# Kernel optimization log

Hardware: AMD Instinct MI355X
Metric: run time of the kernel (lower is better)

Reference implementation:

```python
import jax, jax.numpy as jnp
import numpy as np

N = 50000        # nodes
E = 800000       # edges (avg degree 16)
H = 128          # hidden_channels
R = 6            # num_radial
SH = 3           # spin_hidden_channels


def _linear_params(key, out_dim, in_dim):
    # torch Linear default init: U(-1/sqrt(in), 1/sqrt(in)) for weight and bias
    kw, kb = jax.random.split(key)
    bound = 1.0 / np.sqrt(in_dim)
    W = jax.random.uniform(kw, (out_dim, in_dim), minval=-bound, maxval=bound, dtype=jnp.float32)
    b = jax.random.uniform(kb, (out_dim,), minval=-bound, maxval=bound, dtype=jnp.float32)
    return W, b


def setup_inputs() -> dict:
    key = jax.random.key(0)
    ks = jax.random.split(key, 9)
    x = jax.random.randint(ks[0], (N,), 0, 95)                       # atom types
    s = jax.random.randint(ks[1], (N,), 0, 3)                        # spin class in {0,1,2} == (spin + 1)
    rbf = jax.random.normal(ks[2], (E, R), dtype=jnp.float32)
    i = jax.random.randint(ks[3], (E,), 0, N)
    j = jax.random.randint(ks[4], (E,), 0, N)
    emb_w = jax.random.uniform(ks[5], (95, H), minval=-np.sqrt(3), maxval=np.sqrt(3), dtype=jnp.float32)
    spin_w, spin_b = _linear_params(ks[6], SH, 3)
    rbf_w, rbf_b = _linear_params(ks[7], H, R)
    lin_w, lin_b = _linear_params(ks[8], H, 3 * H + 2 * SH)
    return {"x": x, "s": s, "rbf": rbf, "i": i, "j": j,
            "emb_w": emb_w, "spin_w": spin_w, "spin_b": spin_b,
            "rbf_w": rbf_w, "rbf_b": rbf_b, "lin_w": lin_w, "lin_b": lin_b}


def reference(x, s, rbf, i, j, emb_w, spin_w, spin_b, rbf_w, rbf_b, lin_w, lin_b):
    act = jax.nn.silu
    h = emb_w[x]                                              # [N, H] embedding lookup
    spin_oh = jax.nn.one_hot(s, 3, dtype=spin_w.dtype)        # [N, 3]
    spin_feat = spin_oh @ spin_w.T + spin_b                   # [N, SH]
    r = act(rbf @ rbf_w.T + rbf_b)                            # [E, H]
    # concat order matches torch: [x_i, spin_i, x_j, spin_j, rbf]
    feat = jnp.concatenate([h[i], spin_feat[i], h[j], spin_feat[j], r], axis=-1)  # [E, 3H+2SH]
    return act(feat @ lin_w.T + lin_b)                        # [E, H]
```

## Files before the change

### kernel.cpp

```cpp
#include <hip/hip_runtime.h>
#include <hip/hip_bf16.h>

#define NH   128
#define NR   6
#define NCOL 390
#define TILE_E 128
#define LDK  136
#define NBLK 512

typedef __attribute__((ext_vector_type(8))) short bf16x8;
typedef __attribute__((ext_vector_type(4))) float f32x4;

__device__ __forceinline__ float fast_silu(float v) {
    return v * __builtin_amdgcn_rcpf(1.0f + __expf(-v));
}

__global__ void prep_tables(const float* __restrict__ emb_w,
                            const float* __restrict__ spin_w,
                            const float* __restrict__ spin_b,
                            const float* __restrict__ lin_w,
                            const float* __restrict__ lin_b,
                            float* __restrict__ Ci, float* __restrict__ Cj) {
    int row = blockIdx.x;
    int n   = threadIdx.x;
    bool isJ = row >= 285;
    int rr = isJ ? row - 285 : row;
    int a  = rr / 3;
    int sc = rr % 3;
    const int col0 = isJ ? 131 : 0;
    const int cols = isJ ? 259 : 128;
    const float* wrow = lin_w + (size_t)n * NCOL;
    float acc = isJ ? 0.0f : lin_b[n];
    #pragma unroll 8
    for (int k = 0; k < NH; ++k)
        acc += emb_w[a * NH + k] * wrow[col0 + k];
    #pragma unroll
    for (int c = 0; c < 3; ++c)
        acc += (spin_w[c * 3 + sc] + spin_b[c]) * wrow[cols + c];
    (isJ ? Cj : Ci)[rr * NH + n] = acc;
}

__global__ void prep_w(const float* __restrict__ lin_w, __hip_bfloat16* __restrict__ Wb) {
    int idx = blockIdx.x * 256 + threadIdx.x;
    int n = idx >> 7, k = idx & 127;
    Wb[idx] = __float2bfloat16(lin_w[(size_t)n * NCOL + 262 + k]);
}

__global__ __launch_bounds__(512, 4) void fused_main(
        const int*   __restrict__ x,   const int* __restrict__ s,
        const float* __restrict__ rbf,
        const int*   __restrict__ gi,  const int* __restrict__ gj,
        const float* __restrict__ rbf_w, const float* __restrict__ rbf_b,
        const float* __restrict__ Ci,  const float* __restrict__ Cj,
        const __hip_bfloat16* __restrict__ Wb,
        float* __restrict__ out, int E, int ntiles) {
    __shared__ __align__(16) __hip_bfloat16 w_lds[NH * LDK];
    __shared__ __align__(16) __hip_bfloat16 r_lds[TILE_E * LDK];
    __shared__ float rbf_lds[TILE_E * NR];
    __shared__ int ci_lds[TILE_E], cj_lds[TILE_E];

    const int tid = threadIdx.x;

    float2 srbf = make_float2(0.f, 0.f);
    int sci = 0, scj = 0;

    auto load_tile = [&](int tt) {
        const int en0 = tt * TILE_E;
        if (tid < 384) {
            int nval = (E - en0 >= TILE_E ? TILE_E : E - en0) * NR;
            float2 v = make_float2(0.f, 0.f);
            if (tid * 2 < nval)
                v = ((const float2*)(rbf + (size_t)en0 * NR))[tid];
            srbf = v;
        }
        if (tid >= 384) {
            int e = en0 + (tid - 384); if (e >= E) e = E - 1;
            int ii = gi[e];
            sci = x[ii] * 3 + s[ii];
        }
        if (tid < 128) {
            int e = en0 + tid; if (e >= E) e = E - 1;
            int jj = gj[e];
            scj = x[jj] * 3 + s[jj];
        }
    };

    const int t0 = blockIdx.x;
    const int gstride = gridDim.x;
    load_tile(t0);

    {
        const uint4* src = (const uint4*)Wb;
        #pragma unroll
        for (int it = 0; it < 4; ++it) {
            int l = it * 512 + tid;
            uint4 v = src[l];
            *(uint4*)&w_lds[(l >> 4) * LDK + (l & 15) * 8] = v;
        }
    }

    const int kk = tid & 127;
    const int hi = tid >> 7;
    const float w0 = rbf_w[kk * NR + 0], w1 = rbf_w[kk * NR + 1], w2 = rbf_w[kk * NR + 2];
    const float w3 = rbf_w[kk * NR + 3], w4 = rbf_w[kk * NR + 4], w5 = rbf_w[kk * NR + 5];
    const float bb = rbf_b[kk];

    const int wave   = tid >> 6;
    const int lane   = tid & 63;
    const int lane15 = lane & 15;
    const int quad   = lane >> 4;
    const int e_sub  = wave * 16;
    const int e_row  = e_sub + quad * 4;

    for (int t = t0; t < ntiles; t += gstride) {
        __syncthreads();
        if (tid < 384) ((float2*)rbf_lds)[tid] = srbf;
        if (tid >= 384) ci_lds[tid - 384] = sci;
        if (tid < 128)  cj_lds[tid] = scj;
        __syncthreads();

        #pragma unroll 4
        for (int it = 0; it < 32; ++it) {
            int e = it * 4 + hi;
            const float* re = &rbf_lds[e * NR];
            float a = bb + re[0] * w0 + re[1] * w1 + re[2] * w2
                         + re[3] * w3 + re[4] * w4 + re[5] * w5;
            r_lds[e * LDK + kk] = __float2bfloat16(fast_silu(a));
        }
        __syncthreads();

        bf16x8 afrag[4];
        #pragma unroll
        for (int kt = 0; kt < 4; ++kt)
            afrag[kt] = *(const bf16x8*)&r_lds[(e_sub + lane15) * LDK + kt * 32 + quad * 8];

        const int e0 = t * TILE_E;
        const float* cip[4]; const float* cjp[4]; float* op[4];
        #pragma unroll
        for (int reg = 0; reg < 4; ++reg) {
            cip[reg] = Ci + ci_lds[e_row + reg] * NH + lane15;
            cjp[reg] = Cj + cj_lds[e_row + reg] * NH + lane15;
            op[reg]  = out + (size_t)(e0 + e_row + reg) * NH + lane15;
        }
        const bool tail = (e0 + TILE_E > E);

        int tn = t + gstride;
        if (tn < ntiles) load_tile(tn);

        #pragma unroll
        for (int nt = 0; nt < 8; ++nt) {
            f32x4 acc = {0.f, 0.f, 0.f, 0.f};
            #pragma unroll
            for (int kt = 0; kt < 4; ++kt) {
                bf16x8 bfrag = *(const bf16x8*)&w_lds[(nt * 16 + lane15) * LDK + kt * 32 + quad * 8];
                acc = __builtin_amdgcn_mfma_f32_16x16x32_bf16(afrag[kt], bfrag, acc, 0, 0, 0);
            }
            #pragma unroll
            for (int reg = 0; reg < 4; ++reg) {
                float base = cip[reg][nt * 16] + cjp[reg][nt * 16];
                float v = acc[reg] + base;
                float sv = fast_silu(v);
                if (!tail || (e0 + e_row + reg < E))
                    __builtin_nontemporal_store(sv, op[reg] + nt * 16);
            }
        }
    }
}

extern "C" void kernel_launch(void* const* d_in, const int* in_sizes, int n_in,
                              void* d_out, int out_size, void* d_ws, size_t ws_size,
                              hipStream_t stream) {
    const int*   x      = (const int*)  d_in[0];
    const int*   s      = (const int*)  d_in[1];
    const float* rbf    = (const float*)d_in[2];
    const int*   gi     = (const int*)  d_in[3];
    const int*   gj     = (const int*)  d_in[4];
    const float* emb_w  = (const float*)d_in[5];
    const float* spin_w = (const float*)d_in[6];
    const float* spin_b = (const float*)d_in[7];
    const float* rbf_w  = (const float*)d_in[8];
    const float* rbf_b  = (const float*)d_in[9];
    const float* lin_w  = (const float*)d_in[10];
    const float* lin_b  = (const float*)d_in[11];
    const int E = in_sizes[3];

    float* Ci = (float*)d_ws;
    float* Cj = Ci + 285 * NH;
    __hip_bfloat16* Wb = (__hip_bfloat16*)(Cj + 285 * NH);

    prep_tables<<<570, 128, 0, stream>>>(emb_w, spin_w, spin_b, lin_w, lin_b, Ci, Cj);
    prep_w<<<64, 256, 0, stream>>>(lin_w, Wb);

    int ntiles = (E + TILE_E - 1) / TILE_E;
    int nblk = ntiles < NBLK ? ntiles : NBLK;
    fused_main<<<nblk, 512, 0, stream>>>(x, s, rbf, gi, gj, rbf_w, rbf_b,
                                         Ci, Cj, Wb, (float*)d_out, E, ntiles);
}
```

Measured before the change: 553.9 us.

## Merge prep kernels and read rbf directly from global with register prefetch

Combines the two preprocessing kernels into one launch, and each block now computes the shared embedding dot product once for all three spin classes. In the main kernel the rbf staging through LDS is removed. Each wave reads its edge's six rbf values straight from global memory (wave-uniform addresses, next row prefetched into registers), which drops one barrier per tile. The cost is that rbf loads now sit on the critical path with no cross-tile prefetch.

```diff
diff --git a/kernel.cpp b/kernel.cpp
--- a/kernel.cpp
+++ b/kernel.cpp
@@ -15,35 +15,41 @@
     return v * __builtin_amdgcn_rcpf(1.0f + __expf(-v));
 }
 
-__global__ void prep_tables(const float* __restrict__ emb_w,
-                            const float* __restrict__ spin_w,
-                            const float* __restrict__ spin_b,
-                            const float* __restrict__ lin_w,
-                            const float* __restrict__ lin_b,
-                            float* __restrict__ Ci, float* __restrict__ Cj) {
-    int row = blockIdx.x;
-    int n   = threadIdx.x;
-    bool isJ = row >= 285;
-    int rr = isJ ? row - 285 : row;
-    int a  = rr / 3;
-    int sc = rr % 3;
-    const int col0 = isJ ? 131 : 0;
-    const int cols = isJ ? 259 : 128;
+__global__ void prep_all(const float* __restrict__ emb_w,
+                         const float* __restrict__ spin_w,
+                         const float* __restrict__ spin_b,
+                         const float* __restrict__ lin_w,
+                         const float* __restrict__ lin_b,
+                         float* __restrict__ Ci, float* __restrict__ Cj,
+                         __hip_bfloat16* __restrict__ Wb) {
+    int b = blockIdx.x;
+    int tid = threadIdx.x;
+    if (b >= 190) {
+        int idx = (b - 190) * 128 + tid;
+        int n = idx >> 7, k = idx & 127;
+        Wb[idx] = __float2bfloat16(lin_w[(size_t)n * NCOL + 262 + k]);
+        return;
+    }
+    int side = b & 1;
+    int a    = b >> 1;
+    int n    = tid;
+    const int col0 = side ? 131 : 0;
+    const int cols = side ? 259 : 128;
     const float* wrow = lin_w + (size_t)n * NCOL;
-    float acc = isJ ? 0.0f : lin_b[n];
+    const float* ew   = emb_w + a * NH;
+    float dot = side ? 0.0f : lin_b[n];
     #pragma unroll 8
     for (int k = 0; k < NH; ++k)
-        acc += emb_w[a * NH + k] * wrow[col0 + k];
+        dot += ew[k] * wrow[col0 + k];
+    float* dst = (side ? Cj : Ci) + (size_t)(a * 3) * NH + n;
     #pragma unroll
-    for (int c = 0; c < 3; ++c)
-        acc += (spin_w[c * 3 + sc] + spin_b[c]) * wrow[cols + c];
-    (isJ ? Cj : Ci)[rr * NH + n] = acc;
-}
-
-__global__ void prep_w(const float* __restrict__ lin_w, __hip_bfloat16* __restrict__ Wb) {
-    int idx = blockIdx.x * 256 + threadIdx.x;
-    int n = idx >> 7, k = idx & 127;
-    Wb[idx] = __float2bfloat16(lin_w[(size_t)n * NCOL + 262 + k]);
+    for (int sc = 0; sc < 3; ++sc) {
+        float acc = dot;
+        #pragma unroll
+        for (int c = 0; c < 3; ++c)
+            acc += (spin_w[c * 3 + sc] + spin_b[c]) * wrow[cols + c];
+        dst[(size_t)sc * NH] = acc;
+    }
 }
 
 __global__ __launch_bounds__(512, 4) void fused_main(
@@ -56,23 +62,13 @@
         float* __restrict__ out, int E, int ntiles) {
     __shared__ __align__(16) __hip_bfloat16 w_lds[NH * LDK];
     __shared__ __align__(16) __hip_bfloat16 r_lds[TILE_E * LDK];
-    __shared__ float rbf_lds[TILE_E * NR];
     __shared__ int ci_lds[TILE_E], cj_lds[TILE_E];
 
     const int tid = threadIdx.x;
 
-    float2 srbf = make_float2(0.f, 0.f);
     int sci = 0, scj = 0;
-
-    auto load_tile = [&](int tt) {
+    auto load_idx = [&](int tt) {
         const int en0 = tt * TILE_E;
-        if (tid < 384) {
-            int nval = (E - en0 >= TILE_E ? TILE_E : E - en0) * NR;
-            float2 v = make_float2(0.f, 0.f);
-            if (tid * 2 < nval)
-                v = ((const float2*)(rbf + (size_t)en0 * NR))[tid];
-            srbf = v;
-        }
         if (tid >= 384) {
             int e = en0 + (tid - 384); if (e >= E) e = E - 1;
             int ii = gi[e];
@@ -87,7 +83,7 @@
 
     const int t0 = blockIdx.x;
     const int gstride = gridDim.x;
-    load_tile(t0);
+    load_idx(t0);
 
     {
         const uint4* src = (const uint4*)Wb;
@@ -100,7 +96,7 @@
     }
 
     const int kk = tid & 127;
-    const int hi = tid >> 7;
+    const int hiu = __builtin_amdgcn_readfirstlane(tid >> 7);
     const float w0 = rbf_w[kk * NR + 0], w1 = rbf_w[kk * NR + 1], w2 = rbf_w[kk * NR + 2];
     const float w3 = rbf_w[kk * NR + 3], w4 = rbf_w[kk * NR + 4], w5 = rbf_w[kk * NR + 5];
     const float bb = rbf_b[kk];
@@ -113,19 +109,26 @@
     const int e_row  = e_sub + quad * 4;
 
     for (int t = t0; t < ntiles; t += gstride) {
+        const int e0t = t * TILE_E;
         __syncthreads();
-        if (tid < 384) ((float2*)rbf_lds)[tid] = srbf;
         if (tid >= 384) ci_lds[tid - 384] = sci;
         if (tid < 128)  cj_lds[tid] = scj;
-        __syncthreads();
 
-        #pragma unroll 4
-        for (int it = 0; it < 32; ++it) {
-            int e = it * 4 + hi;
-            const float* re = &rbf_lds[e * NR];
-            float a = bb + re[0] * w0 + re[1] * w1 + re[2] * w2
-                         + re[3] * w3 + re[4] * w4 + re[5] * w5;
-            r_lds[e * LDK + kk] = __float2bfloat16(fast_silu(a));
+        {
+            const int egBase = e0t + hiu * 32;
+            int eg0 = egBase; if (eg0 > E - 1) eg0 = E - 1;
+            const float* rp = rbf + (size_t)eg0 * NR;
+            float c0 = rp[0], c1 = rp[1], c2 = rp[2], c3 = rp[3], c4 = rp[4], c5 = rp[5];
+            #pragma unroll 4
+            for (int it = 0; it < 32; ++it) {
+                int egn = egBase + it + 1; if (egn > E - 1) egn = E - 1;
+                const float* rn = rbf + (size_t)egn * NR;
+                float n0 = rn[0], n1 = rn[1], n2 = rn[2], n3 = rn[3], n4 = rn[4], n5 = rn[5];
+                float a = bb + c0 * w0 + c1 * w1 + c2 * w2
+                             + c3 * w3 + c4 * w4 + c5 * w5;
+                r_lds[(hiu * 32 + it) * LDK + kk] = __float2bfloat16(fast_silu(a));
+                c0 = n0; c1 = n1; c2 = n2; c3 = n3; c4 = n4; c5 = n5;
+            }
         }
         __syncthreads();
 
@@ -134,18 +137,17 @@
         for (int kt = 0; kt < 4; ++kt)
             afrag[kt] = *(const bf16x8*)&r_lds[(e_sub + lane15) * LDK + kt * 32 + quad * 8];
 
-        const int e0 = t * TILE_E;
         const float* cip[4]; const float* cjp[4]; float* op[4];
         #pragma unroll
         for (int reg = 0; reg < 4; ++reg) {
             cip[reg] = Ci + ci_lds[e_row + reg] * NH + lane15;
             cjp[reg] = Cj + cj_lds[e_row + reg] * NH + lane15;
-            op[reg]  = out + (size_t)(e0 + e_row + reg) * NH + lane15;
+            op[reg]  = out + (size_t)(e0t + e_row + reg) * NH + lane15;
         }
-        const bool tail = (e0 + TILE_E > E);
+        const bool tail = (e0t + TILE_E > E);
 
         int tn = t + gstride;
-        if (tn < ntiles) load_tile(tn);
+        if (tn < ntiles) load_idx(tn);
 
         #pragma unroll
         for (int nt = 0; nt < 8; ++nt) {
@@ -160,7 +162,7 @@
                 float base = cip[reg][nt * 16] + cjp[reg][nt * 16];
                 float v = acc[reg] + base;
                 float sv = fast_silu(v);
-                if (!tail || (e0 + e_row + reg < E))
+                if (!tail || (e0t + e_row + reg < E))
                     __builtin_nontemporal_store(sv, op[reg] + nt * 16);
             }
         }
@@ -188,8 +190,7 @@
     float* Cj = Ci + 285 * NH;
     __hip_bfloat16* Wb = (__hip_bfloat16*)(Cj + 285 * NH);
 
-    prep_tables<<<570, 128, 0, stream>>>(emb_w, spin_w, spin_b, lin_w, lin_b, Ci, Cj);
-    prep_w<<<64, 256, 0, stream>>>(lin_w, Wb);
+    prep_all<<<318, 128, 0, stream>>>(emb_w, spin_w, spin_b, lin_w, lin_b, Ci, Cj, Wb);
 
     int ntiles = (E + TILE_E - 1) / TILE_E;
     int nblk = ntiles < NBLK ? ntiles : NBLK;
```

After: 607.4 us. 1.1x slower.
